# Kernel tuning notes

Hardware: AMD Instinct MI355X
Metric: run time of the kernel (lower is better)

## Reference

```python
import jax, jax.numpy as jnp
import numpy as np

HEADS = 8
EPS = 1e-5

def _conv2d(x, w, b):
    # x: (b,c,h,w), w: (out_c,in_c,3,3), padding=1 (SAME)
    y = jax.lax.conv_general_dilated(x, w, (1, 1), ((1, 1), (1, 1)),
                                     dimension_numbers=('NCHW', 'OIHW', 'NCHW'))
    return y + b[None, :, None, None]

def _mcl(x, cw, cb, pw):
    # MultichannelLinear: conv then per-channel pointwise matmul over the h (feature) dim
    y = _conv2d(x, cw, cb)                      # (b,c,in_f,w)
    return jnp.einsum('bchw,cfh->bcfw', y, pw)  # (b,c,out_f,w)

def _ln(x, g, b):
    # MultichannelLayerNorm over the feature (h) axis with per-channel affine
    mu = x.mean(axis=2, keepdims=True)
    var = x.var(axis=2, keepdims=True)
    xn = (x - mu) * jax.lax.rsqrt(var + EPS)
    return xn * g[None, :, :, None] + b[None, :, :, None]

def _rope(t):
    # lucidrains RotaryEmbedding.rotate_queries_or_keys, interleaved pairs; t: (...,w,d)
    d = t.shape[-1]
    w = t.shape[-2]
    inv = 1.0 / (10000.0 ** (jnp.arange(0, d, 2, dtype=jnp.float32) / d))
    ang = jnp.arange(w, dtype=jnp.float32)[:, None] * inv[None, :]   # (w, d/2)
    cos = jnp.repeat(jnp.cos(ang), 2, axis=-1)
    sin = jnp.repeat(jnp.sin(ang), 2, axis=-1)
    t2 = t.reshape(t.shape[:-1] + (d // 2, 2))
    rot = jnp.stack([-t2[..., 1], t2[..., 0]], axis=-1).reshape(t.shape)
    return t * cos + rot * sin

def _split_heads(y, nh):
    b, c, f, w = y.shape
    return y.transpose(0, 1, 3, 2).reshape(b, c, w, nh, f // nh).transpose(0, 1, 3, 2, 4)  # (b,c,nh,w,dh)

def _forward(x, embed_cw, embed_cb, embed_pw, norm1_g, norm1_b,
             q_cw, q_cb, q_pw, k_cw, k_cb, k_pw, v_cw, v_cb, v_pw,
             o_cw, o_cb, o_pw, norm2_g, norm2_b,
             ffn1_cw, ffn1_cb, ffn1_pw, ffn2_cw, ffn2_cb, ffn2_pw):
    b, c_in, hdim, w = x.shape
    h0 = _mcl(x, embed_cw, embed_cb, embed_pw)          # (b,c,feat,w)
    # --- multichannel multihead attention with inline RoPE ---
    xn = _ln(h0, norm1_g, norm1_b)
    q = _rope(_split_heads(_mcl(xn, q_cw, q_cb, q_pw), HEADS))   # (b,c,nh,w,dh)
    k = _rope(_split_heads(_mcl(xn, k_cw, k_cb, k_pw), HEADS))
    v = _split_heads(_mcl(xn, v_cw, v_cb, v_pw), HEADS)
    qk = jnp.einsum('bchqd,bchkd->bchqk', q, k) / jnp.sqrt(jnp.float32(hdim))  # scale by sqrt(h), per source
    a = jnp.einsum('bchqk,bchkd->bchqd', jax.nn.softmax(qk, axis=-1), v)
    bb, cc, nh, ww, dh = a.shape
    a = a.transpose(0, 1, 3, 2, 4).reshape(bb, cc, ww, nh * dh).transpose(0, 1, 3, 2)  # (b,c,feat,w)
    z = _mcl(a, o_cw, o_cb, o_pw)
    h = h0 + z
    # --- squared-ReLU FFN ---
    y = _mcl(_ln(h, norm2_g, norm2_b), ffn1_cw, ffn1_cb, ffn1_pw)
    y = jnp.maximum(y, 0.0) ** 2
    z = _mcl(y, ffn2_cw, ffn2_cb, ffn2_pw)
    h = h + z
    return jnp.concatenate([x, h], axis=1)  # (b, c_in+c_out, feat, w)

def setup_inputs() -> dict:
    key = jax.random.key(0)
    ks = jax.random.split(key, 32)
    C_IN, C, F, W, B, EXP = 8, 4, 1024, 512, 4, 4

    def p(k, shape, fan):
        return jax.random.normal(k, shape, dtype=jnp.float32) * (1.0 / np.sqrt(fan))

    inp = {
        'x': jax.random.normal(ks[0], (B, C_IN, F, W), dtype=jnp.float32),
        'embed_cw': p(ks[1], (C, C_IN, 3, 3), C_IN * 9), 'embed_cb': p(ks[2], (C,), C_IN * 9),
        'embed_pw': p(ks[3], (C, F, F), F),
        'norm1_g': jnp.ones((C, F), jnp.float32), 'norm1_b': jnp.zeros((C, F), jnp.float32),
        'q_cw': p(ks[4], (C, C, 3, 3), C * 9), 'q_cb': p(ks[5], (C,), C * 9), 'q_pw': p(ks[6], (C, F, F), F),
        'k_cw': p(ks[7], (C, C, 3, 3), C * 9), 'k_cb': p(ks[8], (C,), C * 9), 'k_pw': p(ks[9], (C, F, F), F),
        'v_cw': p(ks[10], (C, C, 3, 3), C * 9), 'v_cb': p(ks[11], (C,), C * 9), 'v_pw': p(ks[12], (C, F, F), F),
        'o_cw': p(ks[13], (C, C, 3, 3), C * 9), 'o_cb': p(ks[14], (C,), C * 9), 'o_pw': p(ks[15], (C, F, F), F),
        'norm2_g': jnp.ones((C, F), jnp.float32), 'norm2_b': jnp.zeros((C, F), jnp.float32),
        'ffn1_cw': p(ks[16], (C, C, 3, 3), C * 9), 'ffn1_cb': p(ks[17], (C,), C * 9),
        'ffn1_pw': p(ks[18], (C, F * EXP, F), F),
        'ffn2_cw': p(ks[19], (C, C, 3, 3), C * 9), 'ffn2_cb': p(ks[20], (C,), C * 9),
        'ffn2_pw': p(ks[21], (C, F, F * EXP), F * EXP),
    }
    return inp

def reference(x, embed_cw, embed_cb, embed_pw, norm1_g, norm1_b,
              q_cw, q_cb, q_pw, k_cw, k_cb, k_pw, v_cw, v_cb, v_pw,
              o_cw, o_cb, o_pw, norm2_g, norm2_b,
              ffn1_cw, ffn1_cb, ffn1_pw, ffn2_cw, ffn2_cb, ffn2_pw):
    return _forward(x, embed_cw, embed_cb, embed_pw, norm1_g, norm1_b,
                    q_cw, q_cb, q_pw, k_cw, k_cb, k_pw, v_cw, v_cb, v_pw,
                    o_cw, o_cb, o_pw, norm2_g, norm2_b,
                    ffn1_cw, ffn1_cb, ffn1_pw, ffn2_cw, ffn2_cb, ffn2_pw)
```

## Files before the change

### kernel.cpp

```cpp
#include <hip/hip_runtime.h>

typedef __attribute__((ext_vector_type(8))) short short8;
typedef __attribute__((ext_vector_type(4))) float f32x4;
typedef unsigned int uint;
typedef unsigned short ushort;

#define PLF 524288

__device__ __forceinline__ ushort f2bf(float f) {
  uint u = __float_as_uint(f);
  u += 0x7FFF + ((u >> 16) & 1);
  return (ushort)(u >> 16);
}
__device__ __forceinline__ float bf2f(ushort h) {
  return __uint_as_float(((uint)h) << 16);
}
__device__ __forceinline__ int swzf(int r) { return ((r & 3) ^ ((r >> 2) & 3)); }

#define GLOAD16(gp, lp)                                          \
  __builtin_amdgcn_global_load_lds(                              \
      (const __attribute__((address_space(1))) void*)(gp),       \
      (__attribute__((address_space(3))) void*)(lp), 16, 0, 0)

template <int CDT, int BETA, int RELU2, int MFAST, int ROPE>
__global__ __launch_bounds__(512) void mm2_kernel(
    const ushort* __restrict__ Av, const ushort* __restrict__ Bv, void* __restrict__ Cv,
    int K, int lda, int ldb, int ldc,
    int aDiv, int aMod, long long aS1, long long aS2,
    int bDiv, int bMod, long long bS1, long long bS2,
    int cDiv, int cMod, long long cS1, long long cS2, float alpha)
{
  __shared__ char lds[73728];
  const int nx = gridDim.x, ny = gridDim.y;
  const int nwg = nx * ny * (int)gridDim.z;
  const int o = ((int)blockIdx.z * ny + blockIdx.y) * nx + blockIdx.x;
  const int qd = nwg >> 3, rm = nwg & 7, xcd = o & 7, rot = o >> 3;
  const int wflat = (xcd < rm ? xcd * (qd + 1) : rm * (qd + 1) + (xcd - rm) * qd) + rot;
  int bx, by, bz;
  if (MFAST) { by = wflat % ny; int t2 = wflat / ny; bx = t2 % nx; bz = t2 / nx; }
  else       { bx = wflat % nx; int t2 = wflat / nx; by = t2 % ny; bz = t2 / ny; }
  const int tid = threadIdx.x;
  const long long aOff = (long long)(bz / aDiv) * aS1 + (long long)(bz % aMod) * aS2;
  const long long bOff = (long long)(bz / bDiv) * bS1 + (long long)(bz % bMod) * bS2;
  const long long cOff = (long long)(bz / cDiv) * cS1 + (long long)(bz % cMod) * cS2;
  const int m0 = by * 128, n0 = bx * 256;
  const int lane = tid & 63, wid = tid >> 6;
  const int MOFF = (wid >> 2) * 64, NOFF = (wid & 3) * 64;
  const int u = lane & 15, g = lane >> 4;
  const int sr0 = tid >> 2, sslot = tid & 3;
  const ushort* Ap = Av + aOff;
  const ushort* Bp = Bv + bOff;

#define STAGE2(buf, kt)                                                        \
  {                                                                            \
    {                                                                          \
      const int r = sr0;                                                       \
      const int ss = sslot ^ swzf(r);                                          \
      GLOAD16(Ap + (long long)(m0 + r) * lda + (kt) + ss * 8,                  \
              &lds[(buf) * 24576] + tid * 16);                                 \
    }                                                                          \
    _Pragma("unroll")                                                          \
    for (int half = 0; half < 2; ++half) {                                     \
      const int r = sr0 + 128 * half;                                          \
      const int ss = sslot ^ swzf(r);                                          \
      GLOAD16(Bp + (long long)(n0 + r) * ldb + (kt) + ss * 8,                  \
              &lds[(buf) * 24576 + 8192] + half * 8192 + tid * 16);            \
    }                                                                          \
  }

  f32x4 acc[4][4];
#pragma unroll
  for (int i = 0; i < 4; ++i)
#pragma unroll
    for (int j = 0; j < 4; ++j) acc[i][j] = (f32x4){0.f, 0.f, 0.f, 0.f};

  const int T = K >> 5;
  STAGE2(0, 0);
  if (T > 1) STAGE2(1, 32);
  int rb = 0, sb = 2;
  for (int t = 0; t < T; ++t) {
    if (t + 1 < T) { asm volatile("s_waitcnt vmcnt(3)" ::: "memory"); }
    else           { asm volatile("s_waitcnt vmcnt(0)" ::: "memory"); }
    __builtin_amdgcn_s_barrier();
    __builtin_amdgcn_sched_barrier(0);
    asm volatile("" ::: "memory");
    if (t + 2 < T) STAGE2(sb, (t + 2) * 32);
    const char* Abuf = &lds[rb * 24576];
    const char* Bbuf = &lds[rb * 24576 + 8192];
    short8 af[4], bfr[4];
#pragma unroll
    for (int mi = 0; mi < 4; ++mi) {
      const int r = MOFF + mi * 16 + u;
      af[mi] = *(const short8*)(Abuf + r * 64 + ((g ^ swzf(r)) * 16));
    }
#pragma unroll
    for (int ni = 0; ni < 4; ++ni) {
      const int r = NOFF + ni * 16 + u;
      bfr[ni] = *(const short8*)(Bbuf + r * 64 + ((g ^ swzf(r)) * 16));
    }
    __builtin_amdgcn_s_setprio(1);
#pragma unroll
    for (int mi = 0; mi < 4; ++mi)
#pragma unroll
      for (int ni = 0; ni < 4; ++ni)
        acc[mi][ni] = __builtin_amdgcn_mfma_f32_16x16x32_bf16(af[mi], bfr[ni], acc[mi][ni], 0, 0, 0);
    __builtin_amdgcn_s_setprio(0);
    rb = (rb == 2) ? 0 : rb + 1;
    sb = (sb == 2) ? 0 : sb + 1;
  }
#undef STAGE2

#pragma unroll
  for (int mi = 0; mi < 4; ++mi)
#pragma unroll
    for (int ni = 0; ni < 4; ++ni)
#pragma unroll
      for (int q = 0; q < 4; ++q) {
        const int row = m0 + MOFF + mi * 16 + g * 4 + q;
        const int col = n0 + NOFF + ni * 16 + u;
        float v = acc[mi][ni][q] * alpha;
        if (CDT == 0) {
          float* cp = (float*)Cv + cOff + (long long)row * ldc + col;
          if (BETA) v += *cp;
          *cp = v;
        } else {
          if (ROPE) {
            const int j = (col & 127) >> 1;
            const float infr = __expf((float)j * (-9.210340371976184f / 64.f));
            float sn, cs;
            __sincosf((float)row * infr, &sn, &cs);
            const float part = __shfl_xor(v, 1);
            v = (col & 1) ? fmaf(part, sn, v * cs) : fmaf(-part, sn, v * cs);
          }
          if (RELU2) { v = fmaxf(v, 0.f); v = v * v; }
          ((ushort*)Cv)[cOff + (long long)row * ldc + col] = f2bf(v);
        }
      }
}

template <int CDT, int BETA, int RELU2, int MFAST, int BCVT, int ROPE>
__global__ __launch_bounds__(256) void mm_kernel(
    const void* __restrict__ Av, const void* __restrict__ Bv, void* __restrict__ Cv,
    int K, int lda, int ldb, int ldc,
    int aDiv, int aMod, long long aS1, long long aS2,
    int bDiv, int bMod, long long bS1, long long bS2,
    int cDiv, int cMod, long long cS1, long long cS2, float alpha)
{
  __shared__ char lds[49152];
  const int nx = gridDim.x, ny = gridDim.y;
  const int nwg = nx * ny * (int)gridDim.z;
  const int o = ((int)blockIdx.z * ny + blockIdx.y) * nx + blockIdx.x;
  const int qd = nwg >> 3, rm = nwg & 7, xcd = o & 7, rot = o >> 3;
  const int wflat = (xcd < rm ? xcd * (qd + 1) : rm * (qd + 1) + (xcd - rm) * qd) + rot;
  int bx, by, bz;
  if (MFAST) { by = wflat % ny; int t2 = wflat / ny; bx = t2 % nx; bz = t2 / nx; }
  else       { bx = wflat % nx; int t2 = wflat / nx; by = t2 % ny; bz = t2 / ny; }
  const int tid = threadIdx.x;
  const long long aOff = (long long)(bz / aDiv) * aS1 + (long long)(bz % aMod) * aS2;
  const long long bOff = (long long)(bz / bDiv) * bS1 + (long long)(bz % bMod) * bS2;
  const long long cOff = (long long)(bz / cDiv) * cS1 + (long long)(bz % cMod) * cS2;
  const int m0 = by * 128, n0 = bx * 128;
  const int lane = tid & 63, wid = tid >> 6;
  const int MOFF = (wid >> 1) * 64, NOFF = (wid & 1) * 64;
  const int u = lane & 15, g = lane >> 4;
  const int sr0 = tid >> 2, sslot = tid & 3;
  const ushort* Ap = (const ushort*)Av + aOff;
  const ushort* Bp = (const ushort*)Bv + bOff;
  const float*  Bf = (const float*)Bv + bOff;

#define STAGE(buf, kt)                                                         \
  {                                                                            \
    _Pragma("unroll")                                                          \
    for (int half = 0; half < 2; ++half) {                                     \
      const int r = sr0 + 64 * half;                                           \
      const int ss = sslot ^ swzf(r);                                          \
      GLOAD16(Ap + (long long)(m0 + r) * lda + (kt) + ss * 8,                  \
              &lds[(buf) * 16384] + wid * 1024 + half * 4096);                 \
      if (BCVT == 0) {                                                         \
        GLOAD16(Bp + (long long)(n0 + r) * ldb + (kt) + ss * 8,                \
                &lds[(buf) * 16384 + 8192] + wid * 1024 + half * 4096);        \
      } else {                                                                 \
        const float* srcB = Bf + (long long)(n0 + r) * ldb + (kt) + ss * 8;    \
        float4 x0 = *(const float4*)srcB;                                      \
        float4 x1 = *(const float4*)(srcB + 4);                                \
        short8 h;                                                              \
        h[0] = (short)f2bf(x0.x); h[1] = (short)f2bf(x0.y);                    \
        h[2] = (short)f2bf(x0.z); h[3] = (short)f2bf(x0.w);                    \
        h[4] = (short)f2bf(x1.x); h[5] = (short)f2bf(x1.y);                    \
        h[6] = (short)f2bf(x1.z); h[7] = (short)f2bf(x1.w);                    \
        *(short8*)(&lds[(buf) * 16384 + 8192] + r * 64 + sslot * 16) = h;      \
      }                                                                        \
    }                                                                          \
  }

  f32x4 acc[4][4];
#pragma unroll
  for (int i = 0; i < 4; ++i)
#pragma unroll
    for (int j = 0; j < 4; ++j) acc[i][j] = (f32x4){0.f, 0.f, 0.f, 0.f};

  const int T = K >> 5;
  STAGE(0, 0);
  if (T > 1) STAGE(1, 32);
  int rb = 0, sb = 2;
  for (int t = 0; t < T; ++t) {
    if (BCVT == 0) {
      if (t + 1 < T) { asm volatile("s_waitcnt vmcnt(4)" ::: "memory"); }
      else           { asm volatile("s_waitcnt vmcnt(0)" ::: "memory"); }
    } else {
      asm volatile("s_waitcnt vmcnt(0) lgkmcnt(0)" ::: "memory");
    }
    __builtin_amdgcn_s_barrier();
    __builtin_amdgcn_sched_barrier(0);
    asm volatile("" ::: "memory");
    if (t + 2 < T) STAGE(sb, (t + 2) * 32);
    const char* Abuf = &lds[rb * 16384];
    const char* Bbuf = &lds[rb * 16384 + 8192];
    short8 af[4], bfr[4];
#pragma unroll
    for (int mi = 0; mi < 4; ++mi) {
      const int r = MOFF + mi * 16 + u;
      af[mi] = *(const short8*)(Abuf + r * 64 + ((g ^ swzf(r)) * 16));
    }
#pragma unroll
    for (int ni = 0; ni < 4; ++ni) {
      const int r = NOFF + ni * 16 + u;
      bfr[ni] = *(const short8*)(Bbuf + r * 64 + ((g ^ swzf(r)) * 16));
    }
#pragma unroll
    for (int mi = 0; mi < 4; ++mi)
#pragma unroll
      for (int ni = 0; ni < 4; ++ni)
        acc[mi][ni] = __builtin_amdgcn_mfma_f32_16x16x32_bf16(af[mi], bfr[ni], acc[mi][ni], 0, 0, 0);
    rb = (rb == 2) ? 0 : rb + 1;
    sb = (sb == 2) ? 0 : sb + 1;
  }
#undef STAGE

#pragma unroll
  for (int mi = 0; mi < 4; ++mi)
#pragma unroll
    for (int ni = 0; ni < 4; ++ni)
#pragma unroll
      for (int q = 0; q < 4; ++q) {
        const int row = m0 + MOFF + mi * 16 + g * 4 + q;
        const int col = n0 + NOFF + ni * 16 + u;
        float v = acc[mi][ni][q] * alpha;
        if (CDT == 0) {
          float* cp = (float*)Cv + cOff + (long long)row * ldc + col;
          if (BETA) v += *cp;
          *cp = v;
        } else {
          if (ROPE) {
            const int j = (col & 127) >> 1;
            const float infr = __expf((float)j * (-9.210340371976184f / 64.f));
            float sn, cs;
            __sincosf((float)row * infr, &sn, &cs);
            const float part = __shfl_xor(v, 1);
            v = (col & 1) ? fmaf(part, sn, v * cs) : fmaf(-part, sn, v * cs);
          }
          if (RELU2) { v = fmaxf(v, 0.f); v = v * v; }
          ((ushort*)Cv)[cOff + (long long)row * ldc + col] = f2bf(v);
        }
      }
}

__global__ __launch_bounds__(256) void fattn_kernel(
    const ushort* __restrict__ Qg, const ushort* __restrict__ Kg,
    const ushort* __restrict__ Vg, ushort* __restrict__ Og)
{
  __shared__ char lds[73728];
  const int hb = blockIdx.y, pl = hb >> 3, h = hb & 7;
  const int q0 = blockIdx.x * 64;
  const int tid = threadIdx.x, lane = tid & 63, wv = tid >> 6;
  const int u = lane & 15, g = lane >> 4;
  const ushort* Qh = Qg + (size_t)pl * PLF + h * 128;
  const ushort* Kh = Kg + (size_t)pl * PLF + h * 128;
  const ushort* Vh = Vg + (size_t)pl * PLF + (size_t)(h * 128) * 512;
  ushort* Oh = Og + (size_t)pl * PLF + h * 128;

  short8 qf[4];
  const int qrow = q0 + wv * 16 + u;
#pragma unroll
  for (int dc = 0; dc < 4; ++dc)
    qf[dc] = *(const short8*)(Qh + (size_t)qrow * 1024 + dc * 32 + g * 8);

#define STAGE_KV(buf, kt)                                                     \
  {                                                                           \
    _Pragma("unroll")                                                         \
    for (int it = 0; it < 4; ++it) {                                          \
      const int off = tid * 16 + it * 4096;                                   \
      const int krow = off >> 8, kslot = (off >> 4) & 15;                     \
      GLOAD16(Kh + (size_t)((kt) * 64 + krow) * 1024 +                        \
                  ((kslot ^ ((krow & 7) << 1)) * 8),                          \
              &lds[(buf) * 16384] + off);                                     \
      const int vrow = off >> 7, vslot = (off >> 4) & 7;                      \
      GLOAD16(Vh + (size_t)vrow * 512 + (kt) * 64 + ((vslot ^ (vrow & 7)) * 8), \
              &lds[32768 + (buf) * 16384] + off);                             \
    }                                                                         \
  }

  f32x4 oacc[8];
#pragma unroll
  for (int i = 0; i < 8; ++i) oacc[i] = (f32x4){0.f, 0.f, 0.f, 0.f};
  float m_run = -3.0e38f, l_run = 0.f;

  STAGE_KV(0, 0);
  asm volatile("s_waitcnt vmcnt(0)" ::: "memory");
  __syncthreads();
  int cur = 0;
  for (int kt = 0; kt < 8; ++kt) {
    if (kt + 1 < 8) STAGE_KV(cur ^ 1, kt + 1);
    f32x4 sacc[4];
#pragma unroll
    for (int kn = 0; kn < 4; ++kn) sacc[kn] = (f32x4){0.f, 0.f, 0.f, 0.f};
    __builtin_amdgcn_s_setprio(1);
#pragma unroll
    for (int kn = 0; kn < 4; ++kn) {
      const int r = kn * 16 + u;
      const char* kb = &lds[cur * 16384] + r * 256;
#pragma unroll
      for (int dc = 0; dc < 4; ++dc) {
        short8 kf = *(const short8*)(kb + (((dc * 4 + g) ^ ((u & 7) << 1)) * 16));
        sacc[kn] = __builtin_amdgcn_mfma_f32_16x16x32_bf16(kf, qf[dc], sacc[kn], 0, 0, 0);
      }
    }
    __builtin_amdgcn_s_setprio(0);
    float pm = -3.0e38f;
#pragma unroll
    for (int kn = 0; kn < 4; ++kn)
#pragma unroll
      for (int r = 0; r < 4; ++r) {
        sacc[kn][r] *= 0.03125f;
        pm = fmaxf(pm, sacc[kn][r]);
      }
    pm = fmaxf(pm, __shfl_xor(pm, 16));
    pm = fmaxf(pm, __shfl_xor(pm, 32));
    const float m_new = fmaxf(m_run, pm);
    const float es = __expf(m_run - m_new);
    float psum = 0.f;
    uint pw[4][2];
#pragma unroll
    for (int kn = 0; kn < 4; ++kn) {
      float p0 = __expf(sacc[kn][0] - m_new);
      float p1 = __expf(sacc[kn][1] - m_new);
      float p2 = __expf(sacc[kn][2] - m_new);
      float p3 = __expf(sacc[kn][3] - m_new);
      psum += (p0 + p1) + (p2 + p3);
      pw[kn][0] = (uint)f2bf(p0) | ((uint)f2bf(p1) << 16);
      pw[kn][1] = (uint)f2bf(p2) | ((uint)f2bf(p3) << 16);
    }
    psum += __shfl_xor(psum, 16);
    psum += __shfl_xor(psum, 32);
    l_run = l_run * es + psum;
    m_run = m_new;
    char* pb = &lds[65536 + wv * 2048] + u * 128 + (g & 1) * 8;
#pragma unroll
    for (int kn = 0; kn < 4; ++kn)
      *(uint2*)(pb + (((2 * kn + (g >> 1)) ^ (u & 7)) * 16)) =
          make_uint2(pw[kn][0], pw[kn][1]);
    float es_o[4];
#pragma unroll
    for (int r = 0; r < 4; ++r) es_o[r] = __shfl(es, g * 4 + r);
#pragma unroll
    for (int nd = 0; nd < 8; ++nd)
#pragma unroll
      for (int r = 0; r < 4; ++r) oacc[nd][r] *= es_o[r];
    const char* prd = &lds[65536 + wv * 2048] + u * 128;
    short8 pf[2];
#pragma unroll
    for (int kc = 0; kc < 2; ++kc)
      pf[kc] = *(const short8*)(prd + (((kc * 4 + g) ^ (u & 7)) * 16));
    __builtin_amdgcn_s_setprio(1);
#pragma unroll
    for (int nd = 0; nd < 8; ++nd) {
      const int vr = nd * 16 + u;
      const char* vb = &lds[32768 + cur * 16384] + vr * 128;
#pragma unroll
      for (int kc = 0; kc < 2; ++kc) {
        short8 vf = *(const short8*)(vb + (((kc * 4 + g) ^ (u & 7)) * 16));
        oacc[nd] = __builtin_amdgcn_mfma_f32_16x16x32_bf16(pf[kc], vf, oacc[nd], 0, 0, 0);
      }
    }
    __builtin_amdgcn_s_setprio(0);
    asm volatile("s_waitcnt vmcnt(0)" ::: "memory");
    __syncthreads();
    cur ^= 1;
  }
#undef STAGE_KV
  const float inv_l = 1.f / l_run;
  float inv_o[4];
#pragma unroll
  for (int r = 0; r < 4; ++r) inv_o[r] = __shfl(inv_l, g * 4 + r);
#pragma unroll
  for (int nd = 0; nd < 8; ++nd)
#pragma unroll
    for (int r = 0; r < 4; ++r) {
      const int row = q0 + wv * 16 + g * 4 + r;
      Oh[(size_t)row * 1024 + nd * 16 + u] = f2bf(oacc[nd][r] * inv_o[r]);
    }
}

__global__ __launch_bounds__(256) void cvt_kernel(
    const float4* __restrict__ s, short8* __restrict__ d)
{
  const int i = blockIdx.x * 256 + threadIdx.x;
  const float4 a = s[2 * i], b = s[2 * i + 1];
  short8 h;
  h[0] = (short)f2bf(a.x); h[1] = (short)f2bf(a.y);
  h[2] = (short)f2bf(a.z); h[3] = (short)f2bf(a.w);
  h[4] = (short)f2bf(b.x); h[5] = (short)f2bf(b.y);
  h[6] = (short)f2bf(b.z); h[7] = (short)f2bf(b.w);
  d[i] = h;
}

template <int CIN>
__global__ __launch_bounds__(256) void conv4c_kernel(
    const ushort* __restrict__ in, const float* __restrict__ wt,
    const float* __restrict__ bias, ushort* __restrict__ outp, int log2F)
{
  const int idx = blockIdx.x * 256 + threadIdx.x;
  const int F8m = (1 << (log2F - 3)) - 1;
  const int f8 = idx & F8m;
  const int wp2 = (idx >> (log2F - 3)) & 255;
  const int bb = idx >> (log2F + 5);
  const int w = wp2 * 2;
  const int f0 = f8 << 3;
  float acc[2][4][8];
#pragma unroll
  for (int co = 0; co < 4; ++co) {
    const float bv = bias[co];
#pragma unroll
    for (int j = 0; j < 8; ++j) { acc[0][co][j] = bv; acc[1][co][j] = bv; }
  }
  const bool lok = f8 > 0, rok = f8 < F8m;
#pragma unroll
  for (int ci = 0; ci < CIN; ++ci) {
    const ushort* base = in + (((size_t)(bb * CIN + ci)) << (log2F + 9));
#pragma unroll
    for (int rr = 0; rr < 4; ++rr) {
      const int wr = w - 1 + rr;
      if (wr < 0 || wr > 511) continue;
      const ushort* rp = base + ((size_t)wr << log2F) + f0;
      const short8 cen = *(const short8*)rp;
      float xv[10];
      xv[0] = lok ? bf2f(rp[-1]) : 0.f;
#pragma unroll
      for (int j = 0; j < 8; ++j) xv[j + 1] = bf2f((ushort)cen[j]);
      xv[9] = rok ? bf2f(rp[8]) : 0.f;
#pragma unroll
      for (int co = 0; co < 4; ++co) {
        const float* wp = wt + (co * CIN + ci) * 9;
        if (rr <= 2) {
          const float k0 = wp[rr], k1 = wp[3 + rr], k2 = wp[6 + rr];
#pragma unroll
          for (int j = 0; j < 8; ++j)
            acc[0][co][j] += k0 * xv[j] + k1 * xv[j + 1] + k2 * xv[j + 2];
        }
        if (rr >= 1) {
          const float k0 = wp[rr - 1], k1 = wp[2 + rr], k2 = wp[5 + rr];
#pragma unroll
          for (int j = 0; j < 8; ++j)
            acc[1][co][j] += k0 * xv[j] + k1 * xv[j + 1] + k2 * xv[j + 2];
        }
      }
    }
  }
#pragma unroll
  for (int wo = 0; wo < 2; ++wo)
#pragma unroll
    for (int co = 0; co < 4; ++co) {
      short8 o;
#pragma unroll
      for (int j = 0; j < 8; ++j) o[j] = (short)f2bf(acc[wo][co][j]);
      *(short8*)(outp + (((size_t)(bb * 4 + co)) << (log2F + 9)) +
                 ((size_t)(w + wo) << log2F) + f0) = o;
    }
}

__global__ __launch_bounds__(256) void conv12c_kernel(
    const ushort* __restrict__ in,
    const float* __restrict__ wq, const float* __restrict__ wk, const float* __restrict__ wv,
    const float* __restrict__ bq, const float* __restrict__ bk, const float* __restrict__ bv,
    ushort* __restrict__ outp, int nPl)
{
  const int idx = blockIdx.x * 256 + threadIdx.x;
  const int f8 = idx & 127;
  const int w = (idx >> 7) & 511;
  const int bb = idx >> 16;
  const int f0 = f8 << 3;
  const float* wsel[3] = {wq, wk, wv};
  float acc[12][8];
#pragma unroll
  for (int co = 0; co < 4; ++co) {
    const float b0 = bq[co], b1 = bk[co], b2 = bv[co];
#pragma unroll
    for (int j = 0; j < 8; ++j) {
      acc[co][j] = b0; acc[4 + co][j] = b1; acc[8 + co][j] = b2;
    }
  }
  const bool lok = f8 > 0, rok = f8 < 127;
#pragma unroll
  for (int ci = 0; ci < 4; ++ci) {
    const ushort* base = in + (((size_t)(bb * 4 + ci)) << 19);
#pragma unroll
    for (int dxw = 0; dxw < 3; ++dxw) {
      const int w2 = w + dxw - 1;
      if (w2 < 0 || w2 > 511) continue;
      const ushort* rp = base + ((size_t)w2 << 10) + f0;
      const short8 cen = *(const short8*)rp;
      float xv[10];
      xv[0] = lok ? bf2f(rp[-1]) : 0.f;
#pragma unroll
      for (int j = 0; j < 8; ++j) xv[j + 1] = bf2f((ushort)cen[j]);
      xv[9] = rok ? bf2f(rp[8]) : 0.f;
#pragma unroll
      for (int pj = 0; pj < 3; ++pj)
#pragma unroll
        for (int co = 0; co < 4; ++co) {
          const float* wp = wsel[pj] + (co * 4 + ci) * 9;
          const float k0 = wp[dxw], k1 = wp[3 + dxw], k2 = wp[6 + dxw];
#pragma unroll
          for (int j = 0; j < 8; ++j)
            acc[pj * 4 + co][j] += k0 * xv[j] + k1 * xv[j + 1] + k2 * xv[j + 2];
        }
    }
  }
#pragma unroll
  for (int pj = 0; pj < 3; ++pj)
#pragma unroll
    for (int co = 0; co < 4; ++co) {
      short8 o;
#pragma unroll
      for (int j = 0; j < 8; ++j) o[j] = (short)f2bf(acc[pj * 4 + co][j]);
      *(short8*)(outp + (((size_t)(pj * nPl + bb * 4 + co)) << 19) +
                 ((size_t)w << 10) + f0) = o;
    }
}

__global__ __launch_bounds__(256) void ln_kernel(
    const float* __restrict__ H, const float* __restrict__ gam,
    const float* __restrict__ bet, ushort* __restrict__ XN)
{
  const int wid = threadIdx.x >> 6, lane = threadIdx.x & 63;
  const int row = blockIdx.x * 4 + wid;
  const int c = (row >> 9) & 3;
  const float* xp = H + (size_t)row * 1024;
  float4 v[4];
  float s = 0.f, q = 0.f;
#pragma unroll
  for (int p = 0; p < 4; ++p) {
    v[p] = *(const float4*)(xp + p * 256 + lane * 4);
    s += v[p].x + v[p].y + v[p].z + v[p].w;
    q += v[p].x * v[p].x + v[p].y * v[p].y + v[p].z * v[p].z + v[p].w * v[p].w;
  }
#pragma unroll
  for (int o = 32; o > 0; o >>= 1) { s += __shfl_xor(s, o); q += __shfl_xor(q, o); }
  const float mu = s * (1.f / 1024.f);
  const float var = q * (1.f / 1024.f) - mu * mu;
  const float rs = rsqrtf(var + 1e-5f);
  ushort* op = XN + (size_t)row * 1024;
  const float* gp = gam + c * 1024;
  const float* bp = bet + c * 1024;
#pragma unroll
  for (int p = 0; p < 4; ++p) {
    const int f = p * 256 + lane * 4;
    float4 g4 = *(const float4*)(gp + f);
    float4 b4 = *(const float4*)(bp + f);
    ushort4 o4;
    o4.x = f2bf((v[p].x - mu) * rs * g4.x + b4.x);
    o4.y = f2bf((v[p].y - mu) * rs * g4.y + b4.y);
    o4.z = f2bf((v[p].z - mu) * rs * g4.z + b4.z);
    o4.w = f2bf((v[p].w - mu) * rs * g4.w + b4.w);
    *(ushort4*)(op + f) = o4;
  }
}

__global__ __launch_bounds__(256) void tin_kernel(
    const float* __restrict__ x, ushort* __restrict__ XT,
    float* __restrict__ outp, int planeOff)
{
  __shared__ float t[32][33];
  const int f0 = blockIdx.x * 32, w0 = blockIdx.y * 32;
  const int z = blockIdx.z;
  const int tx = threadIdx.x & 31, ty = threadIdx.x >> 5;
  const int gpl = planeOff + z;
  const int b = gpl >> 3, ch = gpl & 7;
  const float* src = x + (size_t)gpl * PLF;
  float* dst0 = outp + (size_t)(b * 12 + ch) * PLF;
#pragma unroll
  for (int r = 0; r < 32; r += 8) {
    const size_t off = (size_t)(f0 + r + ty) * 512 + w0 + tx;
    const float v = src[off];
    t[r + ty][tx] = v;
    dst0[off] = v;
  }
  __syncthreads();
  ushort* dst = XT + (size_t)z * PLF;
#pragma unroll
  for (int r = 0; r < 32; r += 8) dst[(size_t)(w0 + r + ty) * 1024 + f0 + tx] = f2bf(t[tx][r + ty]);
}

__global__ __launch_bounds__(256) void tout_kernel(
    const float* __restrict__ H, float* __restrict__ out, int b0)
{
  __shared__ float t[32][33];
  const int w0 = blockIdx.x * 32, f0 = blockIdx.y * 32;
  const int p = blockIdx.z;
  const int b = b0 + (p >> 2), c = p & 3;
  const int tx = threadIdx.x & 31, ty = threadIdx.x >> 5;
  const float* src = H + (size_t)p * PLF;
#pragma unroll
  for (int r = 0; r < 32; r += 8) t[r + ty][tx] = src[(size_t)(w0 + r + ty) * 1024 + f0 + tx];
  __syncthreads();
  float* dst = out + (size_t)(b * 12 + 8 + c) * PLF;
#pragma unroll
  for (int r = 0; r < 32; r += 8) dst[(size_t)(f0 + r + ty) * 512 + w0 + tx] = t[tx][r + ty];
}

extern "C" void kernel_launch(void* const* d_in, const int* in_sizes, int n_in,
                              void* d_out, int out_size, void* d_ws, size_t ws_size,
                              hipStream_t stream)
{
  const float* x        = (const float*)d_in[0];
  const float* embed_cw = (const float*)d_in[1];
  const float* embed_cb = (const float*)d_in[2];
  const float* embed_pw = (const float*)d_in[3];
  const float* n1g      = (const float*)d_in[4];
  const float* n1b      = (const float*)d_in[5];
  const float* q_cw     = (const float*)d_in[6];
  const float* q_cb     = (const float*)d_in[7];
  const float* q_pw     = (const float*)d_in[8];
  const float* k_cw     = (const float*)d_in[9];
  const float* k_cb     = (const float*)d_in[10];
  const float* k_pw     = (const float*)d_in[11];
  const float* v_cw     = (const float*)d_in[12];
  const float* v_cb     = (const float*)d_in[13];
  const float* v_pw     = (const float*)d_in[14];
  const float* o_cw     = (const float*)d_in[15];
  const float* o_cb     = (const float*)d_in[16];
  const float* o_pw     = (const float*)d_in[17];
  const float* n2g      = (const float*)d_in[18];
  const float* n2b      = (const float*)d_in[19];
  const float* f1_cw    = (const float*)d_in[20];
  const float* f1_cb    = (const float*)d_in[21];
  const float* f1_pw    = (const float*)d_in[22];
  const float* f2_cw    = (const float*)d_in[23];
  const float* f2_cb    = (const float*)d_in[24];
  const float* f2_pw    = (const float*)d_in[25];
  float* out = (float*)d_out;

  const size_t perB = 50331648ull;
  const int N = (ws_size >= 4 * perB) ? 4 : (ws_size >= 2 * perB) ? 2 : 1;
  const int nP = 4 * N;

  char* base = (char*)d_ws;
  float*  Hf = (float*)base;
  ushort* XT = (ushort*)(base + (size_t)N * 8388608);
  ushort* XN = (ushort*)((char*)XT + (size_t)N * 8388608);
  ushort* Qb = (ushort*)((char*)XN + (size_t)N * 4194304);
  ushort* Kb = (ushort*)((char*)Qb + (size_t)N * 4194304);
  ushort* CT = (ushort*)((char*)Kb + (size_t)N * 4194304);
  ushort* Vb = (ushort*)((char*)CT + (size_t)N * 4194304);
  ushort* SfPb = (ushort*)((char*)Vb + (size_t)N * 4194304);
  ushort* CT3 = SfPb;
  ushort* W8  = SfPb;
  ushort* WQK = XT;
  ushort* MID = XT;
  ushort* f1w = Vb;
  ushort* F2C = Vb;
  ushort* f2w = XT;

  const long long W1 = 1048576;
  const long long W4 = 4194304;
  const long long M1 = 2097152;
  const long long CH3 = (long long)nP * PLF;
  const int GCc1 = N * 128;
  const int GCc4 = N * 512;
  const int GC12 = N * 256;

  for (int b0 = 0; b0 < 4; b0 += N) {
    tin_kernel<<<dim3(32, 16, 8 * N), 256, 0, stream>>>(x, XT, out, b0 * 8);
    conv4c_kernel<8><<<GCc1, 256, 0, stream>>>(XT, embed_cw, embed_cb, CT, 10);
    cvt_kernel<<<2048, 256, 0, stream>>>((const float4*)embed_pw, (short8*)W8);
    mm2_kernel<0, 0, 0, 1, 0><<<dim3(4, 4, nP), 512, 0, stream>>>(
        CT, W8, Hf, 1024, 1024, 1024, 1024,
        1, 1, PLF, 0, 4, 4, 0, W1, 1, 1, PLF, 0, 1.f);
    ln_kernel<<<nP * 128, 256, 0, stream>>>(Hf, n1g, n1b, XN);
    conv12c_kernel<<<GC12, 256, 0, stream>>>(XN, q_cw, k_cw, v_cw,
                                             q_cb, k_cb, v_cb, CT3, nP);
    if (N >= 2) {
      cvt_kernel<<<2048, 256, 0, stream>>>((const float4*)q_pw, (short8*)WQK);
      cvt_kernel<<<2048, 256, 0, stream>>>((const float4*)k_pw, (short8*)(WQK) + 524288);
      mm2_kernel<1, 0, 0, 1, 1><<<dim3(4, 4, 2 * nP), 512, 0, stream>>>(
          CT3, WQK, Qb, 1024, 1024, 1024, 1024,
          1, 1, PLF, 0, nP, 4, 4 * W1, W1, 1, 1, PLF, 0, 1.f);
    } else {
      mm_kernel<1, 0, 0, 1, 1, 1><<<dim3(8, 4, nP), 256, 0, stream>>>(
          CT3, q_pw, Qb, 1024, 1024, 1024, 1024,
          1, 1, PLF, 0, 4, 4, 0, W1, 1, 1, PLF, 0, 1.f);
      mm_kernel<1, 0, 0, 1, 1, 1><<<dim3(8, 4, nP), 256, 0, stream>>>(
          CT3 + CH3, k_pw, Kb, 1024, 1024, 1024, 1024,
          1, 1, PLF, 0, 4, 4, 0, W1, 1, 1, PLF, 0, 1.f);
    }
    cvt_kernel<<<2048, 256, 0, stream>>>((const float4*)v_pw, (short8*)W8);
    mm2_kernel<1, 0, 0, 0, 0><<<dim3(2, 8, nP), 512, 0, stream>>>(
        W8, CT3 + 2 * CH3, Vb, 1024, 1024, 1024, 512,
        4, 4, 0, W1, 1, 1, PLF, 0, 1, 1, PLF, 0, 1.f);
    fattn_kernel<<<dim3(8, nP * 8), 256, 0, stream>>>(Qb, Kb, Vb, Qb);
    conv4c_kernel<4><<<GCc1, 256, 0, stream>>>(Qb, o_cw, o_cb, CT, 10);
    cvt_kernel<<<2048, 256, 0, stream>>>((const float4*)o_pw, (short8*)W8);
    mm2_kernel<0, 1, 0, 1, 0><<<dim3(4, 4, nP), 512, 0, stream>>>(
        CT, W8, Hf, 1024, 1024, 1024, 1024,
        1, 1, PLF, 0, 4, 4, 0, W1, 1, 1, PLF, 0, 1.f);
    ln_kernel<<<nP * 128, 256, 0, stream>>>(Hf, n2g, n2b, XN);
    conv4c_kernel<4><<<GCc1, 256, 0, stream>>>(XN, f1_cw, f1_cb, CT, 10);
    if (N >= 2) {
      cvt_kernel<<<8192, 256, 0, stream>>>((const float4*)f1_pw, (short8*)f1w);
      mm2_kernel<1, 0, 1, 1, 0><<<dim3(16, 4, nP), 512, 0, stream>>>(
          CT, f1w, MID, 1024, 1024, 1024, 4096,
          1, 1, PLF, 0, 4, 4, 0, W4, 1, 1, M1, 0, 1.f);
    } else {
      mm_kernel<1, 0, 1, 1, 1, 0><<<dim3(32, 4, nP), 256, 0, stream>>>(
          CT, f1_pw, MID, 1024, 1024, 1024, 4096,
          1, 1, PLF, 0, 4, 4, 0, W4, 1, 1, M1, 0, 1.f);
    }
    conv4c_kernel<4><<<GCc4, 256, 0, stream>>>(MID, f2_cw, f2_cb, F2C, 12);
    if (N >= 2) {
      cvt_kernel<<<8192, 256, 0, stream>>>((const float4*)f2_pw, (short8*)f2w);
      mm2_kernel<0, 1, 0, 1, 0><<<dim3(4, 4, nP), 512, 0, stream>>>(
          F2C, f2w, Hf, 4096, 4096, 4096, 1024,
          1, 1, M1, 0, 4, 4, 0, W4, 1, 1, PLF, 0, 1.f);
    } else {
      mm_kernel<0, 1, 0, 1, 1, 0><<<dim3(8, 4, nP), 256, 0, stream>>>(
          F2C, f2_pw, Hf, 4096, 4096, 4096, 1024,
          1, 1, M1, 0, 4, 4, 0, W4, 1, 1, PLF, 0, 1.f);
    }
    tout_kernel<<<dim3(16, 32, nP), 256, 0, stream>>>(Hf, out, b0);
  }
}
```

Baseline: 646.9 us.

## Replace shared-tile GEMM with per-wave private LDS staging without block barriers

The 512-thread 128x256 GEMM, where all waves shared A/B tiles through a triple-buffered LDS ring behind block barriers, becomes a 256-thread 128x128 kernel. Each wave now stages its own 64x32 A and B slices into a private double-buffered LDS region, so the s_barrier is gone and each wave syncs only on its own vmcnt. This removes cross-wave barrier stalls at the cost of duplicate global loads, since waves sharing rows or columns each fetch them separately, and of halving the tile's data reuse. Grids double in x to match, and the dead BCVT==0 path of the fallback mm_kernel is removed.

```diff
diff --git a/kernel.cpp b/kernel.cpp
--- a/kernel.cpp
+++ b/kernel.cpp
@@ -23,14 +23,14 @@
       (__attribute__((address_space(3))) void*)(lp), 16, 0, 0)
 
 template <int CDT, int BETA, int RELU2, int MFAST, int ROPE>
-__global__ __launch_bounds__(512) void mm2_kernel(
+__global__ __launch_bounds__(256) void mmw_kernel(
     const ushort* __restrict__ Av, const ushort* __restrict__ Bv, void* __restrict__ Cv,
     int K, int lda, int ldb, int ldc,
     int aDiv, int aMod, long long aS1, long long aS2,
     int bDiv, int bMod, long long bS1, long long bS2,
     int cDiv, int cMod, long long cS1, long long cS2, float alpha)
 {
-  __shared__ char lds[73728];
+  __shared__ char lds[65536];
   const int nx = gridDim.x, ny = gridDim.y;
   const int nwg = nx * ny * (int)gridDim.z;
   const int o = ((int)blockIdx.z * ny + blockIdx.y) * nx + blockIdx.x;
@@ -43,29 +43,25 @@
   const long long aOff = (long long)(bz / aDiv) * aS1 + (long long)(bz % aMod) * aS2;
   const long long bOff = (long long)(bz / bDiv) * bS1 + (long long)(bz % bMod) * bS2;
   const long long cOff = (long long)(bz / cDiv) * cS1 + (long long)(bz % cMod) * cS2;
-  const int m0 = by * 128, n0 = bx * 256;
+  const int m0 = by * 128, n0 = bx * 128;
   const int lane = tid & 63, wid = tid >> 6;
-  const int MOFF = (wid >> 2) * 64, NOFF = (wid & 3) * 64;
+  const int MOFF = (wid >> 1) * 64, NOFF = (wid & 1) * 64;
   const int u = lane & 15, g = lane >> 4;
-  const int sr0 = tid >> 2, sslot = tid & 3;
-  const ushort* Ap = Av + aOff;
-  const ushort* Bp = Bv + bOff;
-
-#define STAGE2(buf, kt)                                                        \
+  char* W = &lds[wid * 16384];
+  const ushort* Apw = Av + aOff + (long long)(m0 + MOFF) * lda;
+  const ushort* Bpw = Bv + bOff + (long long)(n0 + NOFF) * ldb;
+
+#define STAGEW(buf, kt)                                                        \
   {                                                                            \
-    {                                                                          \
-      const int r = sr0;                                                       \
-      const int ss = sslot ^ swzf(r);                                          \
-      GLOAD16(Ap + (long long)(m0 + r) * lda + (kt) + ss * 8,                  \
-              &lds[(buf) * 24576] + tid * 16);                                 \
+    _Pragma("unroll")                                                          \
+    for (int it = 0; it < 4; ++it) {                                           \
+      const int lr = it * 16 + (lane >> 2);                                    \
+      const int ss = (lane & 3) ^ swzf(lr);                                    \
+      GLOAD16(Apw + (long long)lr * lda + (kt) + ss * 8,                       \
+              W + (buf) * 8192 + it * 1024 + lane * 16);                       \
+      GLOAD16(Bpw + (long long)lr * ldb + (kt) + ss * 8,                       \
+              W + (buf) * 8192 + 4096 + it * 1024 + lane * 16);                \
     }                                                                          \
-    _Pragma("unroll")                                                          \
-    for (int half = 0; half < 2; ++half) {                                     \
-      const int r = sr0 + 128 * half;                                          \
-      const int ss = sslot ^ swzf(r);                                          \
-      GLOAD16(Bp + (long long)(n0 + r) * ldb + (kt) + ss * 8,                  \
-              &lds[(buf) * 24576 + 8192] + half * 8192 + tid * 16);            \
-    }                                                                          \
   }
 
   f32x4 acc[4][4];
@@ -75,28 +71,26 @@
     for (int j = 0; j < 4; ++j) acc[i][j] = (f32x4){0.f, 0.f, 0.f, 0.f};
 
   const int T = K >> 5;
-  STAGE2(0, 0);
-  if (T > 1) STAGE2(1, 32);
-  int rb = 0, sb = 2;
+  STAGEW(0, 0);
   for (int t = 0; t < T; ++t) {
-    if (t + 1 < T) { asm volatile("s_waitcnt vmcnt(3)" ::: "memory"); }
-    else           { asm volatile("s_waitcnt vmcnt(0)" ::: "memory"); }
-    __builtin_amdgcn_s_barrier();
+    if (t + 1 < T) {
+      STAGEW((t + 1) & 1, (t + 1) * 32);
+      asm volatile("s_waitcnt vmcnt(8)" ::: "memory");
+    } else {
+      asm volatile("s_waitcnt vmcnt(0)" ::: "memory");
+    }
     __builtin_amdgcn_sched_barrier(0);
-    asm volatile("" ::: "memory");
-    if (t + 2 < T) STAGE2(sb, (t + 2) * 32);
-    const char* Abuf = &lds[rb * 24576];
-    const char* Bbuf = &lds[rb * 24576 + 8192];
+    const char* Wb = W + (t & 1) * 8192;
     short8 af[4], bfr[4];
 #pragma unroll
     for (int mi = 0; mi < 4; ++mi) {
-      const int r = MOFF + mi * 16 + u;
-      af[mi] = *(const short8*)(Abuf + r * 64 + ((g ^ swzf(r)) * 16));
+      const int lr = mi * 16 + u;
+      af[mi] = *(const short8*)(Wb + lr * 64 + ((g ^ swzf(lr)) * 16));
     }
 #pragma unroll
     for (int ni = 0; ni < 4; ++ni) {
-      const int r = NOFF + ni * 16 + u;
-      bfr[ni] = *(const short8*)(Bbuf + r * 64 + ((g ^ swzf(r)) * 16));
+      const int lr = ni * 16 + u;
+      bfr[ni] = *(const short8*)(Wb + 4096 + lr * 64 + ((g ^ swzf(lr)) * 16));
     }
     __builtin_amdgcn_s_setprio(1);
 #pragma unroll
@@ -105,10 +99,8 @@
       for (int ni = 0; ni < 4; ++ni)
         acc[mi][ni] = __builtin_amdgcn_mfma_f32_16x16x32_bf16(af[mi], bfr[ni], acc[mi][ni], 0, 0, 0);
     __builtin_amdgcn_s_setprio(0);
-    rb = (rb == 2) ? 0 : rb + 1;
-    sb = (sb == 2) ? 0 : sb + 1;
-  }
-#undef STAGE2
+  }
+#undef STAGEW
 
 #pragma unroll
   for (int mi = 0; mi < 4; ++mi)
@@ -165,7 +157,6 @@
   const int u = lane & 15, g = lane >> 4;
   const int sr0 = tid >> 2, sslot = tid & 3;
   const ushort* Ap = (const ushort*)Av + aOff;
-  const ushort* Bp = (const ushort*)Bv + bOff;
   const float*  Bf = (const float*)Bv + bOff;
 
 #define STAGE(buf, kt)                                                         \
@@ -176,20 +167,15 @@
       const int ss = sslot ^ swzf(r);                                          \
       GLOAD16(Ap + (long long)(m0 + r) * lda + (kt) + ss * 8,                  \
               &lds[(buf) * 16384] + wid * 1024 + half * 4096);                 \
-      if (BCVT == 0) {                                                         \
-        GLOAD16(Bp + (long long)(n0 + r) * ldb + (kt) + ss * 8,                \
-                &lds[(buf) * 16384 + 8192] + wid * 1024 + half * 4096);        \
-      } else {                                                                 \
-        const float* srcB = Bf + (long long)(n0 + r) * ldb + (kt) + ss * 8;    \
-        float4 x0 = *(const float4*)srcB;                                      \
-        float4 x1 = *(const float4*)(srcB + 4);                                \
-        short8 h;                                                              \
-        h[0] = (short)f2bf(x0.x); h[1] = (short)f2bf(x0.y);                    \
-        h[2] = (short)f2bf(x0.z); h[3] = (short)f2bf(x0.w);                    \
-        h[4] = (short)f2bf(x1.x); h[5] = (short)f2bf(x1.y);                    \
-        h[6] = (short)f2bf(x1.z); h[7] = (short)f2bf(x1.w);                    \
-        *(short8*)(&lds[(buf) * 16384 + 8192] + r * 64 + sslot * 16) = h;      \
-      }                                                                        \
+      const float* srcB = Bf + (long long)(n0 + r) * ldb + (kt) + ss * 8;      \
+      float4 x0 = *(const float4*)srcB;                                        \
+      float4 x1 = *(const float4*)(srcB + 4);                                  \
+      short8 h;                                                                \
+      h[0] = (short)f2bf(x0.x); h[1] = (short)f2bf(x0.y);                      \
+      h[2] = (short)f2bf(x0.z); h[3] = (short)f2bf(x0.w);                      \
+      h[4] = (short)f2bf(x1.x); h[5] = (short)f2bf(x1.y);                      \
+      h[6] = (short)f2bf(x1.z); h[7] = (short)f2bf(x1.w);                      \
+      *(short8*)(&lds[(buf) * 16384 + 8192] + r * 64 + sslot * 16) = h;        \
     }                                                                          \
   }
 
@@ -204,12 +190,7 @@
   if (T > 1) STAGE(1, 32);
   int rb = 0, sb = 2;
   for (int t = 0; t < T; ++t) {
-    if (BCVT == 0) {
-      if (t + 1 < T) { asm volatile("s_waitcnt vmcnt(4)" ::: "memory"); }
-      else           { asm volatile("s_waitcnt vmcnt(0)" ::: "memory"); }
-    } else {
-      asm volatile("s_waitcnt vmcnt(0) lgkmcnt(0)" ::: "memory");
-    }
+    asm volatile("s_waitcnt vmcnt(0) lgkmcnt(0)" ::: "memory");
     __builtin_amdgcn_s_barrier();
     __builtin_amdgcn_sched_barrier(0);
     asm volatile("" ::: "memory");
@@ -683,7 +664,7 @@
     tin_kernel<<<dim3(32, 16, 8 * N), 256, 0, stream>>>(x, XT, out, b0 * 8);
     conv4c_kernel<8><<<GCc1, 256, 0, stream>>>(XT, embed_cw, embed_cb, CT, 10);
     cvt_kernel<<<2048, 256, 0, stream>>>((const float4*)embed_pw, (short8*)W8);
-    mm2_kernel<0, 0, 0, 1, 0><<<dim3(4, 4, nP), 512, 0, stream>>>(
+    mmw_kernel<0, 0, 0, 1, 0><<<dim3(8, 4, nP), 256, 0, stream>>>(
         CT, W8, Hf, 1024, 1024, 1024, 1024,
         1, 1, PLF, 0, 4, 4, 0, W1, 1, 1, PLF, 0, 1.f);
     ln_kernel<<<nP * 128, 256, 0, stream>>>(Hf, n1g, n1b, XN);
@@ -692,7 +673,7 @@
     if (N >= 2) {
       cvt_kernel<<<2048, 256, 0, stream>>>((const float4*)q_pw, (short8*)WQK);
       cvt_kernel<<<2048, 256, 0, stream>>>((const float4*)k_pw, (short8*)(WQK) + 524288);
-      mm2_kernel<1, 0, 0, 1, 1><<<dim3(4, 4, 2 * nP), 512, 0, stream>>>(
+      mmw_kernel<1, 0, 0, 1, 1><<<dim3(8, 4, 2 * nP), 256, 0, stream>>>(
           CT3, WQK, Qb, 1024, 1024, 1024, 1024,
           1, 1, PLF, 0, nP, 4, 4 * W1, W1, 1, 1, PLF, 0, 1.f);
     } else {
@@ -704,20 +685,20 @@
           1, 1, PLF, 0, 4, 4, 0, W1, 1, 1, PLF, 0, 1.f);
     }
     cvt_kernel<<<2048, 256, 0, stream>>>((const float4*)v_pw, (short8*)W8);
-    mm2_kernel<1, 0, 0, 0, 0><<<dim3(2, 8, nP), 512, 0, stream>>>(
+    mmw_kernel<1, 0, 0, 0, 0><<<dim3(4, 8, nP), 256, 0, stream>>>(
         W8, CT3 + 2 * CH3, Vb, 1024, 1024, 1024, 512,
         4, 4, 0, W1, 1, 1, PLF, 0, 1, 1, PLF, 0, 1.f);
     fattn_kernel<<<dim3(8, nP * 8), 256, 0, stream>>>(Qb, Kb, Vb, Qb);
     conv4c_kernel<4><<<GCc1, 256, 0, stream>>>(Qb, o_cw, o_cb, CT, 10);
     cvt_kernel<<<2048, 256, 0, stream>>>((const float4*)o_pw, (short8*)W8);
-    mm2_kernel<0, 1, 0, 1, 0><<<dim3(4, 4, nP), 512, 0, stream>>>(
+    mmw_kernel<0, 1, 0, 1, 0><<<dim3(8, 4, nP), 256, 0, stream>>>(
         CT, W8, Hf, 1024, 1024, 1024, 1024,
         1, 1, PLF, 0, 4, 4, 0, W1, 1, 1, PLF, 0, 1.f);
     ln_kernel<<<nP * 128, 256, 0, stream>>>(Hf, n2g, n2b, XN);
     conv4c_kernel<4><<<GCc1, 256, 0, stream>>>(XN, f1_cw, f1_cb, CT, 10);
     if (N >= 2) {
       cvt_kernel<<<8192, 256, 0, stream>>>((const float4*)f1_pw, (short8*)f1w);
-      mm2_kernel<1, 0, 1, 1, 0><<<dim3(16, 4, nP), 512, 0, stream>>>(
+      mmw_kernel<1, 0, 1, 1, 0><<<dim3(32, 4, nP), 256, 0, stream>>>(
           CT, f1w, MID, 1024, 1024, 1024, 4096,
           1, 1, PLF, 0, 4, 4, 0, W4, 1, 1, M1, 0, 1.f);
     } else {
@@ -728,7 +709,7 @@
     conv4c_kernel<4><<<GCc4, 256, 0, stream>>>(MID, f2_cw, f2_cb, F2C, 12);
     if (N >= 2) {
       cvt_kernel<<<8192, 256, 0, stream>>>((const float4*)f2_pw, (short8*)f2w);
-      mm2_kernel<0, 1, 0, 1, 0><<<dim3(4, 4, nP), 512, 0, stream>>>(
+      mmw_kernel<0, 1, 0, 1, 0><<<dim3(8, 4, nP), 256, 0, stream>>>(
           F2C, f2w, Hf, 4096, 4096, 4096, 1024,
           1, 1, M1, 0, 4, 4, 0, W4, 1, 1, PLF, 0, 1.f);
     } else {
```

New measurement: 754.9 us. 16.7% more time.
